# Performance work log

Measured on AMD Instinct MI355X. Metric: run time of the kernel, lower is better.

The kernel has to match this reference:

```python
import jax, jax.numpy as jnp
import numpy as np

B, CQ, CKV, H, W = 8, 192, 192, 128, 128
NUM_HEADS = 6
KERNEL_SIZES = (7, 9, 11)
K_BRANCHES = 3
H_I = NUM_HEADS // K_BRANCHES          # heads per branch = 2
DIM_PROJ = 192
HEAD_DIM = DIM_PROJ // NUM_HEADS       # 32
BRANCH_CH = DIM_PROJ // K_BRANCHES     # 64 channels per branch (H_I * HEAD_DIM)
SCALE = HEAD_DIM ** -0.5


def _na2d_branch(q, k, v, ksize, rpb):
    """Neighborhood attention 2D, dilation=1, clamped window (NATTEN semantics).
    q,k,v: [B, h, H, W, d]; rpb: [h, 2K-1, 2K-1] or None. Returns [B, h, H, W, d]."""
    Bq, h, Hq, Wq, d = q.shape
    K = ksize
    NS = K // 2
    # window start clamped so every query sees exactly K keys per axis
    rows = jnp.clip(jnp.arange(Hq) - NS, 0, Hq - K)[:, None] + jnp.arange(K)  # [H, K]
    cols = jnp.clip(jnp.arange(Wq) - NS, 0, Wq - K)[:, None] + jnp.arange(K)  # [W, K]
    qs = q * SCALE
    # scores: loop over the K row-taps (small fixed kernel), vectorized over everything else
    attn_rows = []
    for ki in range(K):
        kr = k[:, :, rows[:, ki]]          # [B,h,H,W,d]  gather key rows
        kc = kr[:, :, :, cols]             # [B,h,H,W,K,d] gather key cols
        attn_rows.append(jnp.einsum('bhijd,bhijkd->bhijk', qs, kc))
    attn = jnp.stack(attn_rows, axis=4)    # [B,h,H,W,K,K]
    if rpb is not None:
        # bias index = (key_pos - query_pos) + (K-1) on each axis
        rel_r = rows - jnp.arange(Hq)[:, None] + (K - 1)   # [H,K] in [0, 2K-2]
        rel_c = cols - jnp.arange(Wq)[:, None] + (K - 1)   # [W,K]
        bias = rpb[:, rel_r][:, :, :, rel_c]               # [h,H,K,W,K]
        bias = jnp.transpose(bias, (0, 1, 3, 2, 4))        # [h,H,W,K,K]
        attn = attn + bias[None]
    attn = jax.nn.softmax(attn.reshape(Bq, h, Hq, Wq, K * K), axis=-1)
    attn = attn.reshape(Bq, h, Hq, Wq, K, K)
    out = jnp.zeros((Bq, h, Hq, Wq, d), q.dtype)
    for ki in range(K):
        vr = v[:, :, rows[:, ki]]          # [B,h,H,W,d]
        vc = vr[:, :, :, cols]             # [B,h,H,W,K,d]
        out = out + jnp.einsum('bhijk,bhijkd->bhijd', attn[:, :, :, :, ki], vc)
    return out


def setup_inputs() -> dict:
    key = jax.random.key(0)
    ks = jax.random.split(key, 16)
    inp = {
        'x': jax.random.normal(ks[0], (B, CQ, H, W), jnp.float32),
        'context': jax.random.normal(ks[1], (B, CKV, H, W), jnp.float32),
        'Wq': jax.random.normal(ks[2], (CQ, DIM_PROJ), jnp.float32) * 0.02,
        'bq': jax.random.normal(ks[3], (DIM_PROJ,), jnp.float32) * 0.02,
        'Wk': jax.random.normal(ks[4], (CKV, DIM_PROJ), jnp.float32) * 0.02,
        'bk': jax.random.normal(ks[5], (DIM_PROJ,), jnp.float32) * 0.02,
        'Wv': jax.random.normal(ks[6], (CKV, DIM_PROJ), jnp.float32) * 0.02,
        'bv': jax.random.normal(ks[7], (DIM_PROJ,), jnp.float32) * 0.02,
        'Wo': jax.random.normal(ks[8], (DIM_PROJ, CQ), jnp.float32) * 0.02,
        'bo': jax.random.normal(ks[9], (CQ,), jnp.float32) * 0.02,
        'rpb0': jax.random.normal(ks[10], (H_I, 2 * 7 - 1, 2 * 7 - 1), jnp.float32) * 0.02,
        'rpb1': jax.random.normal(ks[11], (H_I, 2 * 9 - 1, 2 * 9 - 1), jnp.float32) * 0.02,
        'rpb2': jax.random.normal(ks[12], (H_I, 2 * 11 - 1, 2 * 11 - 1), jnp.float32) * 0.02,
    }
    return inp


def reference(x, context, Wq, bq, Wk, bk, Wv, bv, Wo, bo, rpb0, rpb1, rpb2):
    rpbs = (rpb0, rpb1, rpb2)
    xc = jnp.transpose(x, (0, 2, 3, 1))        # [B,H,W,Cq]
    ctx = jnp.transpose(context, (0, 2, 3, 1))  # [B,H,W,Ckv]
    q = xc @ Wq + bq                            # [B,H,W,192]
    k = ctx @ Wk + bk
    v = ctx @ Wv + bv
    outs = []
    for i, ksize in enumerate(KERNEL_SIZES):
        sl = slice(i * BRANCH_CH, (i + 1) * BRANCH_CH)
        def to_heads(t):
            return jnp.transpose(
                t[..., sl].reshape(B, H, W, H_I, HEAD_DIM), (0, 3, 1, 2, 4))
        o = _na2d_branch(to_heads(q), to_heads(k), to_heads(v), ksize, rpbs[i])
        outs.append(jnp.transpose(o, (0, 2, 3, 1, 4)).reshape(B, H, W, BRANCH_CH))
    out = jnp.concatenate(outs, axis=-1) @ Wo + bo   # [B,H,W,Cq]
    return jnp.transpose(out, (0, 3, 1, 2))          # [B,Cq,H,W]
```

## Files before the change

kernel.cpp:

```cpp
#include <hip/hip_runtime.h>
#include <hip/hip_fp16.h>

#define HH 128
#define WW 128
#define NPIX (HH*WW)
#define NB 8
#define NHEADS 6
#define HD 32
#define SCALE 0.17677669529663687f

typedef _Float16 h2 __attribute__((ext_vector_type(2)));
typedef __fp16 g2 __attribute__((ext_vector_type(2)));
typedef _Float16 f16x4 __attribute__((ext_vector_type(4)));
typedef _Float16 f16x8 __attribute__((ext_vector_type(8)));
typedef float f4 __attribute__((ext_vector_type(4)));

#define LDK 40
union U4 { g2 p2[2]; f16x4 v4; };

__global__ __launch_bounds__(512) void prep_wt(
    const float* __restrict__ Wq, const float* __restrict__ Wk,
    const float* __restrict__ Wv, _Float16* __restrict__ wt)
{
    int idx = blockIdx.x * 512 + threadIdx.x;
    int mat = idx / 36864, rem = idx % 36864;
    int k = rem / 192, n = rem % 192;
    const float* W = mat == 0 ? Wq : (mat == 1 ? Wk : Wv);
    wt[(size_t)mat * 36864 + (size_t)n * 192 + k] = (_Float16)W[(size_t)k * 192 + n];
}

__global__ __launch_bounds__(512) void prep_wo(
    const float* __restrict__ Wo, _Float16* __restrict__ woT)
{
    int idx = blockIdx.x * 512 + threadIdx.x;
    int k = idx / 192, n = idx % 192;
    woT[(size_t)n * 192 + k] = (_Float16)Wo[(size_t)k * 192 + n];
}

__global__ __launch_bounds__(512, 2) void proj_mfma(
    const float* __restrict__ x, const float* __restrict__ ctx,
    const _Float16* __restrict__ wt,
    const float* __restrict__ bq, const float* __restrict__ bk, const float* __restrict__ bv,
    _Float16* __restrict__ qh, _Float16* __restrict__ kh, _Float16* __restrict__ vh)
{
    int bid = blockIdx.x;
    int xcd = bid & 7;
    int i = bid >> 3;
    int z, xb;
    if (i < 128) { z = 0; xb = xcd * 128 + i; }
    else { int j = i - 128; z = 1 + (j & 1); xb = xcd * 128 + (j >> 1); }

    const float* A  = (z == 0) ? x : ctx;
    const _Float16* WT = wt + (size_t)z * 36864;
    const float* bias = (z == 0) ? bq : (z == 1 ? bk : bv);
    _Float16* outp = (z == 0) ? qh : (z == 1 ? kh : vh);
    float scale = (z == 0) ? SCALE : 1.f;

    __shared__ _Float16 Ts[128 * 192];

    int t = threadIdx.x;
    int m0 = xb * 128;
    int b  = m0 / NPIX;
    int p0 = m0 % NPIX;
    const float* Ab = A + (size_t)b * 192 * NPIX + p0;

    int lane = t & 63;
    int wid  = t >> 6;
    int wm = wid & 1;
    int wn = wid >> 1;
    int lq = lane & 15;
    int lk = lane >> 4;

    {
        int cq = t >> 7, pp = t & 127;
        int sw = (pp & 7) << 3;
        #pragma unroll
        for (int j = 0; j < 12; j++) {
            int c0 = cq * 48 + j * 4;
            float a0 = Ab[(size_t)(c0)     * NPIX + pp];
            float a1 = Ab[(size_t)(c0 + 1) * NPIX + pp];
            float a2 = Ab[(size_t)(c0 + 2) * NPIX + pp];
            float a3 = Ab[(size_t)(c0 + 3) * NPIX + pp];
            U4 u;
            u.p2[0] = __builtin_amdgcn_cvt_pkrtz(a0, a1);
            u.p2[1] = __builtin_amdgcn_cvt_pkrtz(a2, a3);
            *(f16x4*)&Ts[pp * 192 + (c0 ^ sw)] = u.v4;
        }
    }
    __syncthreads();

    f4 acc[12] = {};
    #pragma unroll
    for (int ks = 0; ks < 6; ks++) {
        f16x8 wf[3];
        #pragma unroll
        for (int ni = 0; ni < 3; ni++)
            wf[ni] = *(const f16x8*)&WT[(size_t)(wn * 48 + ni * 16 + lq) * 192 + ks * 32 + lk * 8];
        #pragma unroll
        for (int mi = 0; mi < 4; mi++) {
            int pix = wm * 64 + mi * 16 + lq;
            f16x8 pfr = *(const f16x8*)&Ts[pix * 192 + ((ks * 32 + lk * 8) ^ ((pix & 7) << 3))];
            #pragma unroll
            for (int ni = 0; ni < 3; ni++)
                acc[mi * 3 + ni] = __builtin_amdgcn_mfma_f32_16x16x32_f16(wf[ni], pfr, acc[mi * 3 + ni], 0, 0, 0);
        }
    }
    __syncthreads();

    #pragma unroll
    for (int mi = 0; mi < 4; mi++) {
        int pix = wm * 64 + mi * 16 + lq;
        int sw = (pix & 7) << 3;
        #pragma unroll
        for (int ni = 0; ni < 3; ni++) {
            int n0 = wn * 48 + ni * 16 + lk * 4;
            f4 v = acc[mi * 3 + ni];
            f4 bb = *(const f4*)&bias[n0];
            U4 u;
            u.p2[0] = __builtin_amdgcn_cvt_pkrtz((v[0] + bb[0]) * scale, (v[1] + bb[1]) * scale);
            u.p2[1] = __builtin_amdgcn_cvt_pkrtz((v[2] + bb[2]) * scale, (v[3] + bb[3]) * scale);
            *(f16x4*)&Ts[pix * 192 + (n0 ^ sw)] = u.v4;
        }
    }
    __syncthreads();

    {
        int p2 = t >> 2, qc = t & 3;
        int sw = (p2 & 7) << 3;
        #pragma unroll
        for (int g = 0; g < 6; g++) {
            f16x8 val = *(const f16x8*)&Ts[p2 * 192 + ((g * 32 + qc * 8) ^ sw)];
            *(f16x8*)(outp + ((size_t)(b * NHEADS + g) * NPIX + p0 + p2) * HD + qc * 8) = val;
        }
    }
}

#define NA2D_SMEM 68352

template<int K>
__device__ __forceinline__ void na2d_tile(
    const _Float16* __restrict__ qh, const _Float16* __restrict__ kh,
    const _Float16* __restrict__ vh, const float* __restrict__ rpb,
    _Float16* __restrict__ ah, char* smem, int b, int g_head, int hi, int ty, int tx)
{
    constexpr int NS = K / 2;
    constexpr int RW = 2 * K - 1;
    _Float16* Vt = (_Float16*)smem;
    float* rpbs = (float*)(smem + 66560);

    int t = threadIdx.x;
    size_t plane = (size_t)(b * NHEADS + g_head) * NPIX;
    int h0 = ty * 16, w0 = tx * 16;
    int rmin = min(max(h0 - NS, 0), HH - K);
    int rtop = min(max(h0 + 15 - NS, 0), HH - K);
    int rows_n = rtop + K - rmin;
    int cwin0 = min(max(w0 - NS, 0), WW - K);
    int ctop = min(max(w0 + 15 - NS, 0), WW - K);
    int cols_n = ctop + K - cwin0;

    for (int i = t; i < RW * RW; i += 512) rpbs[i] = rpb[(size_t)hi * RW * RW + i];

    int ntask = rows_n * 128;
    for (int idx = t; idx < ntask; idx += 512) {
        int row = idx >> 7;
        int key = (idx >> 2) & 31;
        int dc  = idx & 3;
        f16x8 vvv = {0,0,0,0,0,0,0,0};
        if (key < cols_n) {
            size_t pix = plane + (size_t)(rmin + row) * WW + (cwin0 + key);
            vvv = *(const f16x8*)&vh[pix * HD + dc * 8];
        }
        int m = 8 * ((key & 15) >> 2) + 4 * (key >> 4) + (key & 3);
        #pragma unroll
        for (int j = 0; j < 8; j++)
            Vt[row * 1280 + (dc * 8 + j) * LDK + m] = vvv[j];
    }
    __syncthreads();

    int lane = t & 63, wid = t >> 6;
    int lq = lane & 15, lg = lane >> 4;
    int wq = w0 + lq;
    int c0q = min(max(wq - NS, 0), WW - K);
    int klo = c0q - cwin0;
    int shiftc = cwin0 - wq + K - 1;
    f4 zf4 = {0.f, 0.f, 0.f, 0.f};

    #pragma unroll 1
    for (int qi = 0; qi < 2; qi++) {
        int qr = wid * 2 + qi;
        int h = h0 + qr;
        int r0q = min(max(h - NS, 0), HH - K);
        int row_base = r0q - rmin;
        f16x8 qf = *(const f16x8*)&qh[(plane + (size_t)h * WW + w0 + lq) * HD + lg * 8];
        f4 acc0 = zf4, acc1 = zf4;
        float lsum = 0.f;

        #pragma unroll 1
        for (int ki = 0; ki < K; ki++) {
            int row = row_base + ki;
            const _Float16* kgrow = kh + (plane + (size_t)(rmin + row) * WW + cwin0) * HD;
            f16x8 a0 = *(const f16x8*)&kgrow[(size_t)lq * HD + lg * 8];
            f16x8 a1 = *(const f16x8*)&kgrow[(size_t)(16 + lq) * HD + lg * 8];
            f4 s0 = __builtin_amdgcn_mfma_f32_16x16x32_f16(a0, qf, zf4, 0, 0, 0);
            f4 s1 = __builtin_amdgcn_mfma_f32_16x16x32_f16(a1, qf, zf4, 0, 0, 0);

            int rel_r = r0q + ki - h + K - 1;
            const float* rrow = rpbs + rel_r * RW;
            float pf[2][4];
            #pragma unroll
            for (int c = 0; c < 2; c++) {
                #pragma unroll
                for (int r = 0; r < 4; r++) {
                    int key_local = c * 16 + 4 * lg + r;
                    int rc = key_local + shiftc;
                    rc = min(max(rc, 0), RW - 1);
                    float biasv = rrow[rc];
                    bool valid = (unsigned)(key_local - klo) < (unsigned)K;
                    float sv = (c ? s1[r] : s0[r]) + biasv;
                    float pv = valid ? __expf(sv) : 0.f;
                    pf[c][r] = pv;
                    lsum += pv;
                }
            }
            union { g2 p[4]; f16x8 v; } P;
            P.p[0] = __builtin_amdgcn_cvt_pkrtz(pf[0][0], pf[0][1]);
            P.p[1] = __builtin_amdgcn_cvt_pkrtz(pf[0][2], pf[0][3]);
            P.p[2] = __builtin_amdgcn_cvt_pkrtz(pf[1][0], pf[1][1]);
            P.p[3] = __builtin_amdgcn_cvt_pkrtz(pf[1][2], pf[1][3]);

            const _Float16* vbase = &Vt[row * 1280 + lg * 8];
            f16x8 b0 = *(const f16x8*)&vbase[lq * LDK];
            f16x8 b1 = *(const f16x8*)&vbase[(16 + lq) * LDK];
            acc0 = __builtin_amdgcn_mfma_f32_16x16x32_f16(P.v, b0, acc0, 0, 0, 0);
            acc1 = __builtin_amdgcn_mfma_f32_16x16x32_f16(P.v, b1, acc1, 0, 0, 0);
        }

        lsum += __shfl_xor(lsum, 16);
        lsum += __shfl_xor(lsum, 32);
        float inv = 1.f / lsum;
        _Float16* obase = ah + (plane + (size_t)h * WW + w0) * HD;
        #pragma unroll
        for (int r = 0; r < 4; r++) {
            float ir = __shfl(inv, 4 * lg + r);
            obase[(4 * lg + r) * HD + lq]      = (_Float16)(acc0[r] * ir);
            obase[(4 * lg + r) * HD + lq + 16] = (_Float16)(acc1[r] * ir);
        }
    }
}

__global__ __launch_bounds__(512) void na2d_mfma(
    const _Float16* __restrict__ qh, const _Float16* __restrict__ kh,
    const _Float16* __restrict__ vh,
    const float* __restrict__ rpb0, const float* __restrict__ rpb1,
    const float* __restrict__ rpb2, _Float16* __restrict__ ah)
{
    extern __shared__ char smem[];
    int bid = blockIdx.x;
    int xcd = bid & 7;
    int i = bid >> 3;
    int phase = i >> 7;
    int j = i & 127;
    int lb = xcd * 128 + j;
    int bz = lb >> 6;
    int tile = lb & 63;
    int b = bz >> 1, hi = bz & 1;
    int ty = tile >> 3, tx = tile & 7;
    if (phase == 0)      na2d_tile<7>(qh, kh, vh, rpb0, ah, smem, b, 0 + hi, hi, ty, tx);
    else if (phase == 1) na2d_tile<9>(qh, kh, vh, rpb1, ah, smem, b, 2 + hi, hi, ty, tx);
    else                 na2d_tile<11>(qh, kh, vh, rpb2, ah, smem, b, 4 + hi, hi, ty, tx);
}

__global__ __launch_bounds__(512) void oproj_mfma(
    const _Float16* __restrict__ ah, const _Float16* __restrict__ woT,
    const float* __restrict__ bo, float* __restrict__ outp)
{
    int t = threadIdx.x;
    int m0 = blockIdx.x * 128;
    int b  = m0 / NPIX;
    int p0 = m0 % NPIX;

    int lane = t & 63;
    int wid  = t >> 6;
    int wm = wid & 1;
    int wn = wid >> 1;
    int lr = lane & 15;
    int lk = lane >> 4;

    f4 acc[4][3] = {};

    #pragma unroll
    for (int ks = 0; ks < 6; ks++) {
        const _Float16* abase = ah + (size_t)(b * NHEADS + ks) * NPIX * HD;
        f16x8 af[4], bf[3];
        #pragma unroll
        for (int mi = 0; mi < 4; mi++)
            af[mi] = *(const f16x8*)&abase[(size_t)(p0 + wm * 64 + mi * 16 + lr) * HD + lk * 8];
        #pragma unroll
        for (int ni = 0; ni < 3; ni++)
            bf[ni] = *(const f16x8*)&woT[(size_t)(wn * 48 + ni * 16 + lr) * 192 + ks * 32 + lk * 8];
        #pragma unroll
        for (int mi = 0; mi < 4; mi++)
            #pragma unroll
            for (int ni = 0; ni < 3; ni++)
                acc[mi][ni] = __builtin_amdgcn_mfma_f32_16x16x32_f16(af[mi], bf[ni], acc[mi][ni], 0, 0, 0);
    }

    #pragma unroll
    for (int ni = 0; ni < 3; ni++) {
        int n = wn * 48 + ni * 16 + lr;
        float bb = bo[n];
        float* obase = outp + ((size_t)b * 192 + n) * NPIX + p0 + wm * 64;
        #pragma unroll
        for (int mi = 0; mi < 4; mi++) {
            f4 v = acc[mi][ni];
            v[0] += bb; v[1] += bb; v[2] += bb; v[3] += bb;
            *(f4*)&obase[mi * 16 + lk * 4] = v;
        }
    }
}

extern "C" void kernel_launch(void* const* d_in, const int* in_sizes, int n_in,
                              void* d_out, int out_size, void* d_ws, size_t ws_size,
                              hipStream_t stream) {
    const float* x    = (const float*)d_in[0];
    const float* ctx  = (const float*)d_in[1];
    const float* Wq   = (const float*)d_in[2];
    const float* bq   = (const float*)d_in[3];
    const float* Wk   = (const float*)d_in[4];
    const float* bk   = (const float*)d_in[5];
    const float* Wv   = (const float*)d_in[6];
    const float* bv   = (const float*)d_in[7];
    const float* Wo   = (const float*)d_in[8];
    const float* bo   = (const float*)d_in[9];
    const float* rpb0 = (const float*)d_in[10];
    const float* rpb1 = (const float*)d_in[11];
    const float* rpb2 = (const float*)d_in[12];

    size_t N = (size_t)NB * NHEADS * NPIX * HD;
    _Float16* qh = (_Float16*)d_ws;
    _Float16* kh = qh + N;
    _Float16* vh = kh + N;
    _Float16* ah = vh + N;
    float* outp = (float*)d_out;

    _Float16* wt  = (_Float16*)d_out + N;
    _Float16* woT = qh;

    (void)hipFuncSetAttribute((const void*)na2d_mfma,
                              hipFuncAttributeMaxDynamicSharedMemorySize, NA2D_SMEM);

    prep_wt<<<216, 512, 0, stream>>>(Wq, Wk, Wv, wt);
    proj_mfma<<<3072, 512, 0, stream>>>(x, ctx, wt, bq, bk, bv, qh, kh, vh);
    na2d_mfma<<<3072, 512, NA2D_SMEM, stream>>>(qh, kh, vh, rpb0, rpb1, rpb2, ah);
    prep_wo<<<72, 512, 0, stream>>>(Wo, woT);
    oproj_mfma<<<1024, 512, 0, stream>>>(ah, woT, bo, outp);
}
```

Before: 249.2 us.

## Fuse K and V projections per block to reuse staged context tile

The projection kernel now computes both K and V from a single staged context tile per block, so the grid shrinks from 3072 to 2048 blocks and the fp32 context is read from global memory once instead of twice. K/V results are written directly from registers to global memory, skipping the shared-memory transpose stage. The input staging loop is rebatched to issue 32 and then 16 loads before converting, and launch bounds are raised to 4 blocks per SM. The trade-offs are register pressure from the higher occupancy hint, and less coalesced direct f16x4 stores for K/V.

```diff
diff --git a/kernel.cpp b/kernel.cpp
--- a/kernel.cpp
+++ b/kernel.cpp
@@ -37,7 +37,7 @@
     woT[(size_t)n * 192 + k] = (_Float16)Wo[(size_t)k * 192 + n];
 }
 
-__global__ __launch_bounds__(512, 2) void proj_mfma(
+__global__ __launch_bounds__(512, 4) void proj_mfma(
     const float* __restrict__ x, const float* __restrict__ ctx,
     const _Float16* __restrict__ wt,
     const float* __restrict__ bq, const float* __restrict__ bk, const float* __restrict__ bv,
@@ -46,15 +46,10 @@
     int bid = blockIdx.x;
     int xcd = bid & 7;
     int i = bid >> 3;
-    int z, xb;
-    if (i < 128) { z = 0; xb = xcd * 128 + i; }
-    else { int j = i - 128; z = 1 + (j & 1); xb = xcd * 128 + (j >> 1); }
-
-    const float* A  = (z == 0) ? x : ctx;
-    const _Float16* WT = wt + (size_t)z * 36864;
-    const float* bias = (z == 0) ? bq : (z == 1 ? bk : bv);
-    _Float16* outp = (z == 0) ? qh : (z == 1 ? kh : vh);
-    float scale = (z == 0) ? SCALE : 1.f;
+    bool is_q = (i < 128);
+    int xb = xcd * 128 + (is_q ? i : i - 128);
+
+    const float* A = is_q ? x : ctx;
 
     __shared__ _Float16 Ts[128 * 192];
 
@@ -74,63 +69,120 @@
     {
         int cq = t >> 7, pp = t & 127;
         int sw = (pp & 7) << 3;
-        #pragma unroll
-        for (int j = 0; j < 12; j++) {
-            int c0 = cq * 48 + j * 4;
-            float a0 = Ab[(size_t)(c0)     * NPIX + pp];
-            float a1 = Ab[(size_t)(c0 + 1) * NPIX + pp];
-            float a2 = Ab[(size_t)(c0 + 2) * NPIX + pp];
-            float a3 = Ab[(size_t)(c0 + 3) * NPIX + pp];
-            U4 u;
-            u.p2[0] = __builtin_amdgcn_cvt_pkrtz(a0, a1);
-            u.p2[1] = __builtin_amdgcn_cvt_pkrtz(a2, a3);
-            *(f16x4*)&Ts[pp * 192 + (c0 ^ sw)] = u.v4;
+        {
+            float ra[32];
+            #pragma unroll
+            for (int j = 0; j < 32; j++)
+                ra[j] = Ab[(size_t)(cq * 48 + j) * NPIX + pp];
+            __builtin_amdgcn_sched_barrier(0);
+            #pragma unroll
+            for (int j4 = 0; j4 < 8; j4++) {
+                int c0 = cq * 48 + j4 * 4;
+                U4 u;
+                u.p2[0] = __builtin_amdgcn_cvt_pkrtz(ra[j4 * 4],     ra[j4 * 4 + 1]);
+                u.p2[1] = __builtin_amdgcn_cvt_pkrtz(ra[j4 * 4 + 2], ra[j4 * 4 + 3]);
+                *(f16x4*)&Ts[pp * 192 + (c0 ^ sw)] = u.v4;
+            }
+        }
+        {
+            float ra[16];
+            #pragma unroll
+            for (int j = 0; j < 16; j++)
+                ra[j] = Ab[(size_t)(cq * 48 + 32 + j) * NPIX + pp];
+            __builtin_amdgcn_sched_barrier(0);
+            #pragma unroll
+            for (int j4 = 0; j4 < 4; j4++) {
+                int c0 = cq * 48 + 32 + j4 * 4;
+                U4 u;
+                u.p2[0] = __builtin_amdgcn_cvt_pkrtz(ra[j4 * 4],     ra[j4 * 4 + 1]);
+                u.p2[1] = __builtin_amdgcn_cvt_pkrtz(ra[j4 * 4 + 2], ra[j4 * 4 + 3]);
+                *(f16x4*)&Ts[pp * 192 + (c0 ^ sw)] = u.v4;
+            }
         }
     }
     __syncthreads();
 
-    f4 acc[12] = {};
-    #pragma unroll
-    for (int ks = 0; ks < 6; ks++) {
-        f16x8 wf[3];
-        #pragma unroll
-        for (int ni = 0; ni < 3; ni++)
-            wf[ni] = *(const f16x8*)&WT[(size_t)(wn * 48 + ni * 16 + lq) * 192 + ks * 32 + lk * 8];
+    if (is_q) {
+        const _Float16* WT = wt;
+        f4 acc[12] = {};
+        #pragma unroll
+        for (int ks = 0; ks < 6; ks++) {
+            f16x8 wf[3];
+            #pragma unroll
+            for (int ni = 0; ni < 3; ni++)
+                wf[ni] = *(const f16x8*)&WT[(size_t)(wn * 48 + ni * 16 + lq) * 192 + ks * 32 + lk * 8];
+            #pragma unroll
+            for (int mi = 0; mi < 4; mi++) {
+                int pix = wm * 64 + mi * 16 + lq;
+                f16x8 pfr = *(const f16x8*)&Ts[pix * 192 + ((ks * 32 + lk * 8) ^ ((pix & 7) << 3))];
+                #pragma unroll
+                for (int ni = 0; ni < 3; ni++)
+                    acc[mi * 3 + ni] = __builtin_amdgcn_mfma_f32_16x16x32_f16(wf[ni], pfr, acc[mi * 3 + ni], 0, 0, 0);
+            }
+        }
+        __syncthreads();
+
         #pragma unroll
         for (int mi = 0; mi < 4; mi++) {
             int pix = wm * 64 + mi * 16 + lq;
-            f16x8 pfr = *(const f16x8*)&Ts[pix * 192 + ((ks * 32 + lk * 8) ^ ((pix & 7) << 3))];
-            #pragma unroll
-            for (int ni = 0; ni < 3; ni++)
-                acc[mi * 3 + ni] = __builtin_amdgcn_mfma_f32_16x16x32_f16(wf[ni], pfr, acc[mi * 3 + ni], 0, 0, 0);
-        }
-    }
-    __syncthreads();
-
-    #pragma unroll
-    for (int mi = 0; mi < 4; mi++) {
-        int pix = wm * 64 + mi * 16 + lq;
-        int sw = (pix & 7) << 3;
-        #pragma unroll
-        for (int ni = 0; ni < 3; ni++) {
-            int n0 = wn * 48 + ni * 16 + lk * 4;
-            f4 v = acc[mi * 3 + ni];
-            f4 bb = *(const f4*)&bias[n0];
-            U4 u;
-            u.p2[0] = __builtin_amdgcn_cvt_pkrtz((v[0] + bb[0]) * scale, (v[1] + bb[1]) * scale);
-            u.p2[1] = __builtin_amdgcn_cvt_pkrtz((v[2] + bb[2]) * scale, (v[3] + bb[3]) * scale);
-            *(f16x4*)&Ts[pix * 192 + (n0 ^ sw)] = u.v4;
-        }
-    }
-    __syncthreads();
-
-    {
+            int sw = (pix & 7) << 3;
+            #pragma unroll
+            for (int ni = 0; ni < 3; ni++) {
+                int n0 = wn * 48 + ni * 16 + lk * 4;
+                f4 v = acc[mi * 3 + ni];
+                f4 bb = *(const f4*)&bq[n0];
+                U4 u;
+                u.p2[0] = __builtin_amdgcn_cvt_pkrtz((v[0] + bb[0]) * SCALE, (v[1] + bb[1]) * SCALE);
+                u.p2[1] = __builtin_amdgcn_cvt_pkrtz((v[2] + bb[2]) * SCALE, (v[3] + bb[3]) * SCALE);
+                *(f16x4*)&Ts[pix * 192 + (n0 ^ sw)] = u.v4;
+            }
+        }
+        __syncthreads();
+
         int p2 = t >> 2, qc = t & 3;
         int sw = (p2 & 7) << 3;
         #pragma unroll
         for (int g = 0; g < 6; g++) {
             f16x8 val = *(const f16x8*)&Ts[p2 * 192 + ((g * 32 + qc * 8) ^ sw)];
-            *(f16x8*)(outp + ((size_t)(b * NHEADS + g) * NPIX + p0 + p2) * HD + qc * 8) = val;
+            *(f16x8*)(qh + ((size_t)(b * NHEADS + g) * NPIX + p0 + p2) * HD + qc * 8) = val;
+        }
+    } else {
+        #pragma unroll
+        for (int out = 0; out < 2; out++) {
+            const _Float16* WT = wt + (size_t)(1 + out) * 36864;
+            const float* bias = out == 0 ? bk : bv;
+            _Float16* outp = out == 0 ? kh : vh;
+            f4 acc[12] = {};
+            #pragma unroll
+            for (int ks = 0; ks < 6; ks++) {
+                f16x8 wf[3];
+                #pragma unroll
+                for (int ni = 0; ni < 3; ni++)
+                    wf[ni] = *(const f16x8*)&WT[(size_t)(wn * 48 + ni * 16 + lq) * 192 + ks * 32 + lk * 8];
+                #pragma unroll
+                for (int mi = 0; mi < 4; mi++) {
+                    int pix = wm * 64 + mi * 16 + lq;
+                    f16x8 pfr = *(const f16x8*)&Ts[pix * 192 + ((ks * 32 + lk * 8) ^ ((pix & 7) << 3))];
+                    #pragma unroll
+                    for (int ni = 0; ni < 3; ni++)
+                        acc[mi * 3 + ni] = __builtin_amdgcn_mfma_f32_16x16x32_f16(wf[ni], pfr, acc[mi * 3 + ni], 0, 0, 0);
+                }
+            }
+            #pragma unroll
+            for (int mi = 0; mi < 4; mi++) {
+                int p = p0 + wm * 64 + mi * 16 + lq;
+                #pragma unroll
+                for (int ni = 0; ni < 3; ni++) {
+                    int n0 = wn * 48 + ni * 16 + lk * 4;
+                    int g = n0 >> 5, d0 = n0 & 31;
+                    f4 v = acc[mi * 3 + ni];
+                    f4 bb = *(const f4*)&bias[n0];
+                    U4 u;
+                    u.p2[0] = __builtin_amdgcn_cvt_pkrtz(v[0] + bb[0], v[1] + bb[1]);
+                    u.p2[1] = __builtin_amdgcn_cvt_pkrtz(v[2] + bb[2], v[3] + bb[3]);
+                    *(f16x4*)(outp + ((size_t)(b * NHEADS + g) * NPIX + p) * HD + d0) = u.v4;
+                }
+            }
         }
     }
 }
@@ -350,7 +402,7 @@
                               hipFuncAttributeMaxDynamicSharedMemorySize, NA2D_SMEM);
 
     prep_wt<<<216, 512, 0, stream>>>(Wq, Wk, Wv, wt);
-    proj_mfma<<<3072, 512, 0, stream>>>(x, ctx, wt, bq, bk, bv, qh, kh, vh);
+    proj_mfma<<<2048, 512, 0, stream>>>(x, ctx, wt, bq, bk, bv, qh, kh, vh);
     na2d_mfma<<<3072, 512, NA2D_SMEM, stream>>>(qh, kh, vh, rpb0, rpb1, rpb2, ah);
     prep_wo<<<72, 512, 0, stream>>>(Wo, woT);
     oproj_mfma<<<1024, 512, 0, stream>>>(ah, woT, bo, outp);
```

Measured after the change: 253.9 us. No clear change (+1.9%).
